# Optimization experiments

Measured on AMD Instinct MI355X. Metric: run time of the kernel, lower is better.

## Reference

```python
import jax, jax.numpy as jnp
import numpy as np


def setup_inputs() -> dict:
    key = jax.random.key(0)
    ks = jax.random.split(key, 8)
    B, C, L = 8, 512, 2048
    Cr = C // 8
    s = 1.0 / np.sqrt(C)
    return {
        "x": jax.random.normal(ks[0], (B, C, L), dtype=jnp.float32),
        "wq": jax.random.normal(ks[1], (Cr, C), dtype=jnp.float32) * s,
        "bq": jnp.zeros((Cr,), dtype=jnp.float32),
        "wk": jax.random.normal(ks[2], (Cr, C), dtype=jnp.float32) * s,
        "bk": jnp.zeros((Cr,), dtype=jnp.float32),
        "wv": jax.random.normal(ks[3], (C, C), dtype=jnp.float32) * s,
        "bv": jnp.zeros((C,), dtype=jnp.float32),
        "gamma": jnp.zeros((1,), dtype=jnp.float32),
    }


def reference(x, wq, bq, wk, bk, wv, bv, gamma):
    # 1x1 conv == pointwise linear over channels: [B,C,L] -> [B,Cout,L]
    q = jnp.einsum('oc,bcl->bol', wq, x) + bq[None, :, None]   # [B,C/8,L]
    k = jnp.einsum('oc,bcl->bol', wk, x) + bk[None, :, None]   # [B,C/8,L]
    v = jnp.einsum('oc,bcl->bol', wv, x) + bv[None, :, None]   # [B,C,L]
    # energy[b,i,j] = sum_d q[b,d,i] * k[b,d,j]  (no 1/sqrt(d) scaling, per source)
    energy = jnp.einsum('bdi,bdj->bij', q, k)                  # [B,L,L]
    attn = jax.nn.softmax(energy, axis=-1)                     # softmax over j
    # out[b,c,i] = sum_j v[b,c,j] * attn[b,i,j]
    out = jnp.einsum('bcj,bij->bci', v, attn)                  # [B,C,L]
    return gamma[0] * out + x
```

## Files before the change

### kernel.cpp

```cpp
#include <hip/hip_runtime.h>
#include <cmath>

#define LL  2048
#define CIN 512
#define CR  64
#define LOG2E 1.44269504088896340736f
#define M0   48.0f

typedef __bf16 bf16x8 __attribute__((ext_vector_type(8)));
typedef float f32x4 __attribute__((ext_vector_type(4)));
typedef unsigned int u32;
typedef unsigned short u16;
typedef unsigned long long u64;

__device__ __forceinline__ u16 f2bf(float f) {
  return __builtin_bit_cast(u16, (__bf16)f);
}
__device__ __forceinline__ bf16x8 ld8(const u16* p) {
  return *reinterpret_cast<const bf16x8*>(p);
}
__device__ __forceinline__ f32x4 mfma16(bf16x8 a, bf16x8 b, f32x4 c) {
  return __builtin_amdgcn_mfma_f32_16x16x32_bf16(a, b, c, 0, 0, 0);
}
__device__ __forceinline__ float fexp2(float x) {
#if __has_builtin(__builtin_amdgcn_exp2f)
  return __builtin_amdgcn_exp2f(x);
#else
  return exp2f(x);
#endif
}
__device__ __forceinline__ void barrier_lds_only() {
  asm volatile("s_waitcnt lgkmcnt(0)" ::: "memory");
  __builtin_amdgcn_s_barrier();
  asm volatile("" ::: "memory");
}
__device__ __forceinline__ u16* pp(u16* base, int row, int col) {
  u32 off = ((u32)row << 8) + ((u32)col << 1);
  off ^= ((u32)(row & 7) << 4);
  return (u16*)((char*)base + off);
}
__device__ __forceinline__ const u16* ppc(const u16* base, int row, int col) {
  u32 off = ((u32)row << 8) + ((u32)col << 1);
  off ^= ((u32)(row & 7) << 4);
  return (const u16*)((const char*)base + off);
}


__global__ void cvt_weights(const float* __restrict__ wq, const float* __restrict__ wk,
                            const float* __restrict__ wv, u16* __restrict__ out) {
  int i = blockIdx.x * 256 + threadIdx.x;
  float val; int rel; u16* dst;
  if (i < CR * CIN)          { rel = i;                val = wq[rel] * LOG2E; dst = out; }
  else if (i < 2 * CR * CIN) { rel = i - CR * CIN;     val = wk[rel];         dst = out + CR * CIN; }
  else                       { rel = i - 2 * CR * CIN; val = wv[rel];         dst = out + 2 * CR * CIN; }
  const int o = rel >> 9, c = rel & 511;
  dst[(size_t)((o >> 4) * 16 + (c >> 5)) * 512 + ((c & 31) >> 3) * 128 + (o & 15) * 8 + (c & 7)] = f2bf(val);
}

__global__ __launch_bounds__(256) void xpose(const float* __restrict__ X, u16* __restrict__ xF) {
  __shared__ u16 tile[64 * 72];
  const int bb = blockIdx.z;
  const int c0 = blockIdx.y * 64;
  const int i0 = blockIdx.x * 64;
  const int t  = threadIdx.x;
  const float* Xb = X + (size_t)bb * CIN * LL;
  u32* tile32 = (u32*)tile;
#pragma unroll
  for (int r = 0; r < 8; r++) {
    int idx = t + r * 256;
    int cw = idx >> 6, i = idx & 63;
    float f0 = Xb[(size_t)(c0 + 2 * cw) * LL + i0 + i];
    float f1 = Xb[(size_t)(c0 + 2 * cw + 1) * LL + i0 + i];
    tile32[i * 36 + cw] = (u32)f2bf(f0) | ((u32)f2bf(f1) << 16);
  }
  __syncthreads();
  const int w = t >> 6, l = t & 63;
  u16* out = xF + (size_t)bb * LL * CIN;
  const int igrp0 = i0 >> 4, cg0 = c0 >> 5;
#pragma unroll
  for (int q = 0; q < 2; q++) {
    const int f  = w * 2 + q;
    const int fi = f >> 1, fc = f & 1;
    bf16x8 vv = ld8(&tile[(fi * 16 + (l & 15)) * 72 + fc * 32 + (l >> 4) * 8]);
    *(bf16x8*)(out + (size_t)((igrp0 + fi) * 16 + cg0 + fc) * 512 + l * 8) = vv;
  }
}

__global__ __launch_bounds__(256, 4) void proj_all(
    const u16* __restrict__ xF, const u16* __restrict__ wqF, const u16* __restrict__ wkF,
    const u16* __restrict__ wvF, const float* __restrict__ bq, const float* __restrict__ bk,
    const float* __restrict__ bv,
    u16* __restrict__ qT, u16* __restrict__ kF, u16* __restrict__ vF)
{
  const int bb = blockIdx.z;
  const int bx = blockIdx.x;
  const int t  = threadIdx.x;
  const int w  = t >> 6, l = t & 63;
  const int li = l & 15, g = l >> 4;
  const u16* xFb = xF + (size_t)bb * LL * CIN;

  if (bx < 64) {
    const int i0 = bx * 32;
    const int igrp0 = bx * 2;
    const int proj = w >> 1;
    const int oh = (w & 1) * 32;
    const int rg0 = oh >> 4;
    const u16* Wf = proj ? wkF : wqF;
    const float* Bs = proj ? bk : bq;
    const float bscale = proj ? 1.0f : LOG2E;

    f32x4 acc[2][2];
#pragma unroll
    for (int mt = 0; mt < 2; mt++)
#pragma unroll
      for (int nt = 0; nt < 2; nt++) acc[mt][nt] = f32x4{0.f, 0.f, 0.f, 0.f};

    bf16x8 aA[2], bA[2], aB[2], bB[2];
#define LDQK(af, bf2, cg)                                                  \
    do {                                                                   \
      af[0]  = ld8(xFb + (size_t)((igrp0    ) * 16 + (cg)) * 512 + l * 8); \
      af[1]  = ld8(xFb + (size_t)((igrp0 + 1) * 16 + (cg)) * 512 + l * 8); \
      bf2[0] = ld8(Wf  + (size_t)((rg0      ) * 16 + (cg)) * 512 + l * 8); \
      bf2[1] = ld8(Wf  + (size_t)((rg0   + 1) * 16 + (cg)) * 512 + l * 8); \
    } while (0)

    LDQK(aA, bA, 0);
#pragma unroll
    for (int cg = 0; cg < 16; cg += 2) {
      LDQK(aB, bB, cg + 1);
#pragma unroll
      for (int mt = 0; mt < 2; mt++)
#pragma unroll
        for (int nt = 0; nt < 2; nt++) acc[mt][nt] = mfma16(aA[mt], bA[nt], acc[mt][nt]);
      if (cg + 2 < 16) LDQK(aA, bA, cg + 2);
#pragma unroll
      for (int mt = 0; mt < 2; mt++)
#pragma unroll
        for (int nt = 0; nt < 2; nt++) acc[mt][nt] = mfma16(aB[mt], bB[nt], acc[mt][nt]);
    }
#undef LDQK

    if (proj == 0) {
      u16* Out = qT + (size_t)bb * LL * CR;
#pragma unroll
      for (int mt = 0; mt < 2; mt++)
#pragma unroll
        for (int nt = 0; nt < 2; nt++) {
          const int o = oh + nt * 16 + li;
          const float bias = Bs[o] * bscale;
#pragma unroll
          for (int r = 0; r < 4; r++) {
            const int i = i0 + mt * 16 + g * 4 + r;
            Out[(size_t)i * CR + o] = f2bf(acc[mt][nt][r] + bias);
          }
        }
    } else {
      u16* Out = kF + (size_t)bb * LL * CR;
      const int kk = oh >> 5;
#pragma unroll
      for (int mt = 0; mt < 2; mt++) {
        const int jgrp = (i0 >> 4) + mt;
#pragma unroll
        for (int nt = 0; nt < 2; nt++) {
          const int o = oh + nt * 16 + li;
          const float bias = Bs[o] * bscale;
          const int shi = (nt * 2 + (li >> 3)) * 16;
          const int e   = li & 7;
#pragma unroll
          for (int r = 0; r < 4; r++) {
            const int slot = shi + g * 4 + r;
            Out[(size_t)(jgrp * 2 + kk) * 512 + slot * 8 + e] = f2bf(acc[mt][nt][r] + bias);
          }
        }
      }
    }
  } else {
    const int vx = bx - 64;
    const int i0 = (vx & 31) * 64;
    const int o0 = (vx >> 5) * 64;
    const int igrp_v = (i0 >> 4) + w;
    const int rgv0 = o0 >> 4;

    f32x4 acc[4];
#pragma unroll
    for (int mt = 0; mt < 4; mt++) acc[mt] = f32x4{0.f, 0.f, 0.f, 0.f};

    bf16x8 xA, aA[4], xB, aB[4];
#define LDV(xf, af, cg)                                                      \
    do {                                                                     \
      xf    = ld8(xFb + (size_t)(igrp_v * 16 + (cg)) * 512 + l * 8);         \
      af[0] = ld8(wvF + (size_t)((rgv0    ) * 16 + (cg)) * 512 + l * 8);     \
      af[1] = ld8(wvF + (size_t)((rgv0 + 1) * 16 + (cg)) * 512 + l * 8);     \
      af[2] = ld8(wvF + (size_t)((rgv0 + 2) * 16 + (cg)) * 512 + l * 8);     \
      af[3] = ld8(wvF + (size_t)((rgv0 + 3) * 16 + (cg)) * 512 + l * 8);     \
    } while (0)

    LDV(xA, aA, 0);
#pragma unroll
    for (int cg = 0; cg < 16; cg += 2) {
      LDV(xB, aB, cg + 1);
#pragma unroll
      for (int mt = 0; mt < 4; mt++) acc[mt] = mfma16(aA[mt], xA, acc[mt]);
      if (cg + 2 < 16) LDV(xA, aA, cg + 2);
#pragma unroll
      for (int mt = 0; mt < 4; mt++) acc[mt] = mfma16(aB[mt], xB, acc[mt]);
    }
#undef LDV

    u16* Vb = vF + (size_t)bb * CIN * LL;
    const int jg2 = (i0 >> 5) + (w >> 1);
    const int gg  = (w & 1) * 2 + (li >> 3);
    const int e   = li & 7;
#pragma unroll
    for (int mt = 0; mt < 4; mt++) {
      const int cgrp = (o0 >> 4) + mt;
#pragma unroll
      for (int r = 0; r < 4; r++) {
        const int o = o0 + mt * 16 + g * 4 + r;
        const int slot = gg * 16 + (g * 4 + r);
        Vb[(size_t)(cgrp * 64 + jg2) * 512 + slot * 8 + e] = f2bf(acc[mt][r] + bv[o]);
      }
    }
  }
}

__global__ __launch_bounds__(256, 2) void attn_mfma(
    const u16* __restrict__ qT, const u16* __restrict__ kF, const u16* __restrict__ vF,
    const float* __restrict__ X, const float* __restrict__ Gamma, float* __restrict__ Y,
    int nb)
{
  __shared__ u16 Pls[2][64 * 128];
  __shared__ float lsb[4][64];
  const int bid  = blockIdx.x;
  const int bb   = bid % nb;
  const int tile = bid / nb;
  const int i0   = (tile >> 1) * 64;
  const int ch   = (tile & 1) * 256;
  const int t    = threadIdx.x;
  const int w    = t >> 6, l = t & 63;
  const int li   = l & 15, g = l >> 4;
  const int c0   = ch + w * 64;
  const u16* qTb = qT + (size_t)bb * LL * CR;
  const u16* kFb = kF + (size_t)bb * LL * CR;
  const u16* vFb = vF + (size_t)bb * CIN * LL;
  const int  cg0 = c0 >> 4;

  bf16x8 qf[4][2];
#pragma unroll
  for (int nt = 0; nt < 4; nt++)
#pragma unroll
    for (int kk = 0; kk < 2; kk++)
      qf[nt][kk] = ld8(qTb + (size_t)(i0 + nt * 16 + li) * CR + kk * 32 + g * 8);

  f32x4 acc[4][4];
#pragma unroll
  for (int mC = 0; mC < 4; mC++)
#pragma unroll
    for (int ni = 0; ni < 4; ni++) acc[mC][ni] = f32x4{0.f, 0.f, 0.f, 0.f};
  float lsum[4] = {0.f, 0.f, 0.f, 0.f};

#pragma unroll 1
  for (int jt = 0; jt < LL; jt += 128) {
    u16* Pbuf = Pls[(jt >> 7) & 1];

    bf16x8 kf[2][2];
#pragma unroll
    for (int mt = 0; mt < 2; mt++)
#pragma unroll
      for (int kk = 0; kk < 2; kk++)
        kf[mt][kk] = ld8(kFb + (size_t)((((jt >> 4) + w * 2 + mt) * 2 + kk)) * 512 + l * 8);
    bf16x8 va[4], vb2[4];
#pragma unroll
    for (int mC = 0; mC < 4; mC++)
      va[mC] = ld8(vFb + (size_t)((cg0 + mC) * 64 + (jt >> 5)) * 512 + l * 8);

    f32x4 s[2][4];
#pragma unroll
    for (int mt = 0; mt < 2; mt++)
#pragma unroll
      for (int nt = 0; nt < 4; nt++) {
        s[mt][nt] = mfma16(kf[mt][0], qf[nt][0], f32x4{0.f, 0.f, 0.f, 0.f});
        s[mt][nt] = mfma16(kf[mt][1], qf[nt][1], s[mt][nt]);
      }

#pragma unroll
    for (int mt = 0; mt < 2; mt++) {
      const int colb = w * 32 + mt * 16 + g * 4;
#pragma unroll
      for (int nt = 0; nt < 4; nt++) {
        const float e0 = fexp2(s[mt][nt][0] - M0);
        const float e1 = fexp2(s[mt][nt][1] - M0);
        const float e2 = fexp2(s[mt][nt][2] - M0);
        const float e3 = fexp2(s[mt][nt][3] - M0);
        lsum[nt] += (e0 + e1) + (e2 + e3);
        u32 lo = (u32)f2bf(e0) | ((u32)f2bf(e1) << 16);
        u32 hi = (u32)f2bf(e2) | ((u32)f2bf(e3) << 16);
        *(u64*)pp(Pbuf, nt * 16 + li, colb) = ((u64)hi << 32) | lo;
      }
    }

    barrier_lds_only();

#pragma unroll
    for (int mC = 0; mC < 4; mC++)
      vb2[mC] = ld8(vFb + (size_t)((cg0 + mC) * 64 + (jt >> 5) + 1) * 512 + l * 8);
    {
      bf16x8 pf[4];
#pragma unroll
      for (int ni = 0; ni < 4; ni++) pf[ni] = ld8(ppc(Pbuf, ni * 16 + li, 0 * 32 + g * 8));
      __builtin_amdgcn_s_setprio(1);
#pragma unroll
      for (int mC = 0; mC < 4; mC++)
#pragma unroll
        for (int ni = 0; ni < 4; ni++) acc[mC][ni] = mfma16(va[mC], pf[ni], acc[mC][ni]);
      __builtin_amdgcn_s_setprio(0);
    }
#pragma unroll
    for (int mC = 0; mC < 4; mC++)
      va[mC] = ld8(vFb + (size_t)((cg0 + mC) * 64 + (jt >> 5) + 2) * 512 + l * 8);
    {
      bf16x8 pf[4];
#pragma unroll
      for (int ni = 0; ni < 4; ni++) pf[ni] = ld8(ppc(Pbuf, ni * 16 + li, 1 * 32 + g * 8));
      __builtin_amdgcn_s_setprio(1);
#pragma unroll
      for (int mC = 0; mC < 4; mC++)
#pragma unroll
        for (int ni = 0; ni < 4; ni++) acc[mC][ni] = mfma16(vb2[mC], pf[ni], acc[mC][ni]);
      __builtin_amdgcn_s_setprio(0);
    }
#pragma unroll
    for (int mC = 0; mC < 4; mC++)
      vb2[mC] = ld8(vFb + (size_t)((cg0 + mC) * 64 + (jt >> 5) + 3) * 512 + l * 8);
    {
      bf16x8 pf[4];
#pragma unroll
      for (int ni = 0; ni < 4; ni++) pf[ni] = ld8(ppc(Pbuf, ni * 16 + li, 2 * 32 + g * 8));
      __builtin_amdgcn_s_setprio(1);
#pragma unroll
      for (int mC = 0; mC < 4; mC++)
#pragma unroll
        for (int ni = 0; ni < 4; ni++) acc[mC][ni] = mfma16(va[mC], pf[ni], acc[mC][ni]);
      __builtin_amdgcn_s_setprio(0);
    }
    {
      bf16x8 pf[4];
#pragma unroll
      for (int ni = 0; ni < 4; ni++) pf[ni] = ld8(ppc(Pbuf, ni * 16 + li, 3 * 32 + g * 8));
      __builtin_amdgcn_s_setprio(1);
#pragma unroll
      for (int mC = 0; mC < 4; mC++)
#pragma unroll
        for (int ni = 0; ni < 4; ni++) acc[mC][ni] = mfma16(vb2[mC], pf[ni], acc[mC][ni]);
      __builtin_amdgcn_s_setprio(0);
    }
  }

#pragma unroll
  for (int nt = 0; nt < 4; nt++) {
    lsum[nt] += __shfl_xor(lsum[nt], 16);
    lsum[nt] += __shfl_xor(lsum[nt], 32);
  }
  if (g == 0) {
#pragma unroll
    for (int nt = 0; nt < 4; nt++) lsb[w][nt * 16 + li] = lsum[nt];
  }
  __syncthreads();
  float linv[4];
#pragma unroll
  for (int nt = 0; nt < 4; nt++) {
    const int i = nt * 16 + li;
    linv[nt] = 1.0f / (lsb[0][i] + lsb[1][i] + lsb[2][i] + lsb[3][i]);
  }

  const float gamma = Gamma[0];
  const float* Xb = X + (size_t)bb * CIN * LL;
  float*       Yb = Y + (size_t)bb * CIN * LL;
#pragma unroll
  for (int mC = 0; mC < 4; mC++)
#pragma unroll
    for (int ni = 0; ni < 4; ni++)
#pragma unroll
      for (int r = 0; r < 4; r++) {
        const int c = c0 + mC * 16 + g * 4 + r;
        const int i = i0 + ni * 16 + li;
        const size_t off = (size_t)c * LL + i;
        Yb[off] = gamma * acc[mC][ni][r] * linv[ni] + Xb[off];
      }
}

extern "C" void kernel_launch(void* const* d_in, const int* in_sizes, int n_in,
                              void* d_out, int out_size, void* d_ws, size_t ws_size,
                              hipStream_t stream) {
  const float* x  = (const float*)d_in[0];
  const float* wq = (const float*)d_in[1];
  const float* bq = (const float*)d_in[2];
  const float* wk = (const float*)d_in[3];
  const float* bk = (const float*)d_in[4];
  const float* wv = (const float*)d_in[5];
  const float* bv = (const float*)d_in[6];
  const float* gm = (const float*)d_in[7];
  float* y = (float*)d_out;

  u16* wqF = (u16*)d_ws;
  u16* wkF = wqF + (size_t)CR * CIN;
  u16* wvF = wkF + (size_t)CR * CIN;
  u16* dyn = wvF + (size_t)CIN * CIN;
  const size_t wbytes = ((size_t)2 * CR * CIN + (size_t)CIN * CIN) * 2;
  const size_t perb = ((size_t)LL * CIN + 2 * (size_t)LL * CR + (size_t)CIN * LL);
  int nbc = 8;
  while (nbc > 1 && ws_size < wbytes + perb * 2 * (size_t)nbc) nbc >>= 1;

  const dim3 blk(256, 1, 1);
  const int nw = 2 * CR * CIN + CIN * CIN;
  hipLaunchKernelGGL(cvt_weights, dim3((nw + 255) / 256), blk, 0, stream, wq, wk, wv, wqF);

  for (int b0 = 0; b0 < 8; b0 += nbc) {
    const int nb = (8 - b0 < nbc) ? (8 - b0) : nbc;
    u16* xF = dyn;
    u16* qT = xF + (size_t)nb * LL * CIN;
    u16* kF = qT + (size_t)nb * LL * CR;
    u16* vF = kF + (size_t)nb * LL * CR;
    const float* xb = x + (size_t)b0 * CIN * LL;
    float*       yb = y + (size_t)b0 * CIN * LL;

    hipLaunchKernelGGL(xpose, dim3(LL / 64, CIN / 64, nb), blk, 0, stream, xb, xF);
    hipLaunchKernelGGL(proj_all, dim3(320, 1, nb), blk, 0, stream,
                       xF, wqF, wkF, wvF, bq, bk, bv, qT, kF, vF);
    hipLaunchKernelGGL(attn_mfma, dim3(64 * nb, 1, 1), blk, 0, stream,
                       qT, kF, vF, xb, gm, yb, nb);
  }
}
```

Before: 95.08 us.

## Use 512-thread attention blocks covering all channels and prefetch K/V across iterations

The attention kernel now runs 8 waves per block, so one block covers all 512 output channels for a 64-query tile. Before, two blocks each handled 256 channels, so each block recomputed the full QK^T and exp. Now each wave computes a 16-column slice of the 128-key score tile, which removes the duplicated softmax work. K fragments and V fragments are software-pipelined with register double-buffering and sched_barriers so next-tile loads overlap the MFMAs. The cost is fewer blocks in the grid (256 instead of 512) and higher register pressure under the 512-thread launch bound, which may reduce occupancy.

Result: faster. 92.29 us (-2.9%).

```diff
diff --git a/kernel.cpp b/kernel.cpp
--- a/kernel.cpp
+++ b/kernel.cpp
@@ -224,33 +224,31 @@
   }
 }
 
-__global__ __launch_bounds__(256, 2) void attn_mfma(
+__global__ __launch_bounds__(512, 2) void attn_mfma(
     const u16* __restrict__ qT, const u16* __restrict__ kF, const u16* __restrict__ vF,
     const float* __restrict__ X, const float* __restrict__ Gamma, float* __restrict__ Y,
     int nb)
 {
   __shared__ u16 Pls[2][64 * 128];
-  __shared__ float lsb[4][64];
+  __shared__ float lsb[8][64];
   const int bid  = blockIdx.x;
   const int bb   = bid % nb;
-  const int tile = bid / nb;
-  const int i0   = (tile >> 1) * 64;
-  const int ch   = (tile & 1) * 256;
+  const int i0   = (bid / nb) * 64;
   const int t    = threadIdx.x;
   const int w    = t >> 6, l = t & 63;
   const int li   = l & 15, g = l >> 4;
-  const int c0   = ch + w * 64;
+  const int c0   = w * 64;
+  const int cg0  = c0 >> 4;
   const u16* qTb = qT + (size_t)bb * LL * CR;
   const u16* kFb = kF + (size_t)bb * LL * CR;
   const u16* vFb = vF + (size_t)bb * CIN * LL;
-  const int  cg0 = c0 >> 4;
 
   bf16x8 qf[4][2];
 #pragma unroll
-  for (int nt = 0; nt < 4; nt++)
+  for (int ni = 0; ni < 4; ni++)
 #pragma unroll
     for (int kk = 0; kk < 2; kk++)
-      qf[nt][kk] = ld8(qTb + (size_t)(i0 + nt * 16 + li) * CR + kk * 32 + g * 8);
+      qf[ni][kk] = ld8(qTb + (size_t)(i0 + ni * 16 + li) * CR + kk * 32 + g * 8);
 
   f32x4 acc[4][4];
 #pragma unroll
@@ -258,119 +256,119 @@
 #pragma unroll
     for (int ni = 0; ni < 4; ni++) acc[mC][ni] = f32x4{0.f, 0.f, 0.f, 0.f};
   float lsum[4] = {0.f, 0.f, 0.f, 0.f};
+
+  bf16x8 kfc[2], kfn[2];
+  kfc[0] = ld8(kFb + (size_t)(w * 2 + 0) * 512 + l * 8);
+  kfc[1] = ld8(kFb + (size_t)(w * 2 + 1) * 512 + l * 8);
+  bf16x8 vA[4], vB[4], vC[4], vD[4];
+#pragma unroll
+  for (int mC = 0; mC < 4; mC++)
+    vA[mC] = ld8(vFb + (size_t)((cg0 + mC) * 64 + 0) * 512 + l * 8);
+#pragma unroll
+  for (int mC = 0; mC < 4; mC++)
+    vB[mC] = ld8(vFb + (size_t)((cg0 + mC) * 64 + 1) * 512 + l * 8);
 
 #pragma unroll 1
   for (int jt = 0; jt < LL; jt += 128) {
     u16* Pbuf = Pls[(jt >> 7) & 1];
-
-    bf16x8 kf[2][2];
-#pragma unroll
-    for (int mt = 0; mt < 2; mt++)
-#pragma unroll
-      for (int kk = 0; kk < 2; kk++)
-        kf[mt][kk] = ld8(kFb + (size_t)((((jt >> 4) + w * 2 + mt) * 2 + kk)) * 512 + l * 8);
-    bf16x8 va[4], vb2[4];
-#pragma unroll
-    for (int mC = 0; mC < 4; mC++)
-      va[mC] = ld8(vFb + (size_t)((cg0 + mC) * 64 + (jt >> 5)) * 512 + l * 8);
-
-    f32x4 s[2][4];
-#pragma unroll
-    for (int mt = 0; mt < 2; mt++)
-#pragma unroll
-      for (int nt = 0; nt < 4; nt++) {
-        s[mt][nt] = mfma16(kf[mt][0], qf[nt][0], f32x4{0.f, 0.f, 0.f, 0.f});
-        s[mt][nt] = mfma16(kf[mt][1], qf[nt][1], s[mt][nt]);
-      }
-
-#pragma unroll
-    for (int mt = 0; mt < 2; mt++) {
-      const int colb = w * 32 + mt * 16 + g * 4;
-#pragma unroll
-      for (int nt = 0; nt < 4; nt++) {
-        const float e0 = fexp2(s[mt][nt][0] - M0);
-        const float e1 = fexp2(s[mt][nt][1] - M0);
-        const float e2 = fexp2(s[mt][nt][2] - M0);
-        const float e3 = fexp2(s[mt][nt][3] - M0);
-        lsum[nt] += (e0 + e1) + (e2 + e3);
-        u32 lo = (u32)f2bf(e0) | ((u32)f2bf(e1) << 16);
-        u32 hi = (u32)f2bf(e2) | ((u32)f2bf(e3) << 16);
-        *(u64*)pp(Pbuf, nt * 16 + li, colb) = ((u64)hi << 32) | lo;
-      }
+    const int jn  = (jt + 128 < LL) ? jt + 128 : 0;
+    const int jg  = jt >> 5;
+    const int jgn = jn >> 5;
+
+    f32x4 s[4];
+#pragma unroll
+    for (int ni = 0; ni < 4; ni++) {
+      s[ni] = mfma16(kfc[0], qf[ni][0], f32x4{0.f, 0.f, 0.f, 0.f});
+      s[ni] = mfma16(kfc[1], qf[ni][1], s[ni]);
+    }
+    kfn[0] = ld8(kFb + (size_t)((((jn >> 4) + w) * 2 + 0)) * 512 + l * 8);
+    kfn[1] = ld8(kFb + (size_t)((((jn >> 4) + w) * 2 + 1)) * 512 + l * 8);
+#pragma unroll
+    for (int mC = 0; mC < 4; mC++)
+      vC[mC] = ld8(vFb + (size_t)((cg0 + mC) * 64 + jg + 2) * 512 + l * 8);
+#pragma unroll
+    for (int mC = 0; mC < 4; mC++)
+      vD[mC] = ld8(vFb + (size_t)((cg0 + mC) * 64 + jg + 3) * 512 + l * 8);
+    __builtin_amdgcn_sched_barrier(0);
+
+    const int colb = w * 16 + g * 4;
+#pragma unroll
+    for (int ni = 0; ni < 4; ni++) {
+      const float e0 = fexp2(s[ni][0] - M0);
+      const float e1 = fexp2(s[ni][1] - M0);
+      const float e2 = fexp2(s[ni][2] - M0);
+      const float e3 = fexp2(s[ni][3] - M0);
+      lsum[ni] += (e0 + e1) + (e2 + e3);
+      u32 lo = (u32)f2bf(e0) | ((u32)f2bf(e1) << 16);
+      u32 hi = (u32)f2bf(e2) | ((u32)f2bf(e3) << 16);
+      *(u64*)pp(Pbuf, ni * 16 + li, colb) = ((u64)hi << 32) | lo;
     }
 
     barrier_lds_only();
 
-#pragma unroll
-    for (int mC = 0; mC < 4; mC++)
-      vb2[mC] = ld8(vFb + (size_t)((cg0 + mC) * 64 + (jt >> 5) + 1) * 512 + l * 8);
-    {
-      bf16x8 pf[4];
-#pragma unroll
-      for (int ni = 0; ni < 4; ni++) pf[ni] = ld8(ppc(Pbuf, ni * 16 + li, 0 * 32 + g * 8));
-      __builtin_amdgcn_s_setprio(1);
-#pragma unroll
-      for (int mC = 0; mC < 4; mC++)
-#pragma unroll
-        for (int ni = 0; ni < 4; ni++) acc[mC][ni] = mfma16(va[mC], pf[ni], acc[mC][ni]);
-      __builtin_amdgcn_s_setprio(0);
-    }
-#pragma unroll
-    for (int mC = 0; mC < 4; mC++)
-      va[mC] = ld8(vFb + (size_t)((cg0 + mC) * 64 + (jt >> 5) + 2) * 512 + l * 8);
-    {
-      bf16x8 pf[4];
-#pragma unroll
-      for (int ni = 0; ni < 4; ni++) pf[ni] = ld8(ppc(Pbuf, ni * 16 + li, 1 * 32 + g * 8));
-      __builtin_amdgcn_s_setprio(1);
-#pragma unroll
-      for (int mC = 0; mC < 4; mC++)
-#pragma unroll
-        for (int ni = 0; ni < 4; ni++) acc[mC][ni] = mfma16(vb2[mC], pf[ni], acc[mC][ni]);
-      __builtin_amdgcn_s_setprio(0);
-    }
-#pragma unroll
-    for (int mC = 0; mC < 4; mC++)
-      vb2[mC] = ld8(vFb + (size_t)((cg0 + mC) * 64 + (jt >> 5) + 3) * 512 + l * 8);
-    {
-      bf16x8 pf[4];
-#pragma unroll
-      for (int ni = 0; ni < 4; ni++) pf[ni] = ld8(ppc(Pbuf, ni * 16 + li, 2 * 32 + g * 8));
-      __builtin_amdgcn_s_setprio(1);
-#pragma unroll
-      for (int mC = 0; mC < 4; mC++)
-#pragma unroll
-        for (int ni = 0; ni < 4; ni++) acc[mC][ni] = mfma16(va[mC], pf[ni], acc[mC][ni]);
-      __builtin_amdgcn_s_setprio(0);
-    }
-    {
-      bf16x8 pf[4];
-#pragma unroll
-      for (int ni = 0; ni < 4; ni++) pf[ni] = ld8(ppc(Pbuf, ni * 16 + li, 3 * 32 + g * 8));
-      __builtin_amdgcn_s_setprio(1);
-#pragma unroll
-      for (int mC = 0; mC < 4; mC++)
-#pragma unroll
-        for (int ni = 0; ni < 4; ni++) acc[mC][ni] = mfma16(vb2[mC], pf[ni], acc[mC][ni]);
-      __builtin_amdgcn_s_setprio(0);
-    }
-  }
-
-#pragma unroll
-  for (int nt = 0; nt < 4; nt++) {
-    lsum[nt] += __shfl_xor(lsum[nt], 16);
-    lsum[nt] += __shfl_xor(lsum[nt], 32);
+    bf16x8 pf[4];
+#pragma unroll
+    for (int ni = 0; ni < 4; ni++) pf[ni] = ld8(ppc(Pbuf, ni * 16 + li, 0 * 32 + g * 8));
+    __builtin_amdgcn_s_setprio(1);
+#pragma unroll
+    for (int mC = 0; mC < 4; mC++)
+#pragma unroll
+      for (int ni = 0; ni < 4; ni++) acc[mC][ni] = mfma16(vA[mC], pf[ni], acc[mC][ni]);
+    __builtin_amdgcn_s_setprio(0);
+#pragma unroll
+    for (int mC = 0; mC < 4; mC++)
+      vA[mC] = ld8(vFb + (size_t)((cg0 + mC) * 64 + jgn + 0) * 512 + l * 8);
+    __builtin_amdgcn_sched_barrier(0);
+#pragma unroll
+    for (int ni = 0; ni < 4; ni++) pf[ni] = ld8(ppc(Pbuf, ni * 16 + li, 1 * 32 + g * 8));
+    __builtin_amdgcn_s_setprio(1);
+#pragma unroll
+    for (int mC = 0; mC < 4; mC++)
+#pragma unroll
+      for (int ni = 0; ni < 4; ni++) acc[mC][ni] = mfma16(vB[mC], pf[ni], acc[mC][ni]);
+    __builtin_amdgcn_s_setprio(0);
+#pragma unroll
+    for (int mC = 0; mC < 4; mC++)
+      vB[mC] = ld8(vFb + (size_t)((cg0 + mC) * 64 + jgn + 1) * 512 + l * 8);
+    __builtin_amdgcn_sched_barrier(0);
+#pragma unroll
+    for (int ni = 0; ni < 4; ni++) pf[ni] = ld8(ppc(Pbuf, ni * 16 + li, 2 * 32 + g * 8));
+    __builtin_amdgcn_s_setprio(1);
+#pragma unroll
+    for (int mC = 0; mC < 4; mC++)
+#pragma unroll
+      for (int ni = 0; ni < 4; ni++) acc[mC][ni] = mfma16(vC[mC], pf[ni], acc[mC][ni]);
+    __builtin_amdgcn_s_setprio(0);
+#pragma unroll
+    for (int ni = 0; ni < 4; ni++) pf[ni] = ld8(ppc(Pbuf, ni * 16 + li, 3 * 32 + g * 8));
+    __builtin_amdgcn_s_setprio(1);
+#pragma unroll
+    for (int mC = 0; mC < 4; mC++)
+#pragma unroll
+      for (int ni = 0; ni < 4; ni++) acc[mC][ni] = mfma16(vD[mC], pf[ni], acc[mC][ni]);
+    __builtin_amdgcn_s_setprio(0);
+
+    kfc[0] = kfn[0];
+    kfc[1] = kfn[1];
+  }
+
+#pragma unroll
+  for (int ni = 0; ni < 4; ni++) {
+    lsum[ni] += __shfl_xor(lsum[ni], 16);
+    lsum[ni] += __shfl_xor(lsum[ni], 32);
   }
   if (g == 0) {
 #pragma unroll
-    for (int nt = 0; nt < 4; nt++) lsb[w][nt * 16 + li] = lsum[nt];
+    for (int ni = 0; ni < 4; ni++) lsb[w][ni * 16 + li] = lsum[ni];
   }
   __syncthreads();
   float linv[4];
 #pragma unroll
-  for (int nt = 0; nt < 4; nt++) {
-    const int i = nt * 16 + li;
-    linv[nt] = 1.0f / (lsb[0][i] + lsb[1][i] + lsb[2][i] + lsb[3][i]);
+  for (int ni = 0; ni < 4; ni++) {
+    const int i = ni * 16 + li;
+    float s8 = lsb[0][i] + lsb[1][i] + lsb[2][i] + lsb[3][i]
+             + lsb[4][i] + lsb[5][i] + lsb[6][i] + lsb[7][i];
+    linv[ni] = 1.0f / s8;
   }
 
   const float gamma = Gamma[0];
@@ -427,7 +425,7 @@
     hipLaunchKernelGGL(xpose, dim3(LL / 64, CIN / 64, nb), blk, 0, stream, xb, xF);
     hipLaunchKernelGGL(proj_all, dim3(320, 1, nb), blk, 0, stream,
                        xF, wqF, wkF, wvF, bq, bk, bv, qT, kF, vF);
-    hipLaunchKernelGGL(attn_mfma, dim3(64 * nb, 1, 1), blk, 0, stream,
+    hipLaunchKernelGGL(attn_mfma, dim3(32 * nb, 1, 1), dim3(512, 1, 1), 0, stream,
                        qT, kF, vF, xb, gm, yb, nb);
   }
 }
```
